# Kernel optimization log

Hardware: AMD Instinct MI355X
Metric: run time of the kernel (lower is better)

The kernel has to match this reference:

```python
import jax, jax.numpy as jnp
import numpy as np

N = 100_000          # NEURON_COUNT (scaled)
INPUT_SIZE = 1024    # input neurons occupy indices [0, INPUT_SIZE)
OUTPUT_SIZE = 256    # output neurons occupy indices [N-OUTPUT_SIZE, N)
E = 10_000_000       # SYNAPSE_RATIO * N
STEPS = 3


def setup_inputs() -> dict:
    key = jax.random.key(0)
    k1, k2, k3, k4, k5 = jax.random.split(key, 5)
    x = jax.random.normal(k1, (INPUT_SIZE,), dtype=jnp.float32)
    synapse_weights = jax.random.normal(k2, (E,), dtype=jnp.float32)
    neuron_biases = jax.random.normal(k3, (N - INPUT_SIZE,), dtype=jnp.float32)
    synapse_src = jax.random.randint(k4, (E,), 0, N, dtype=jnp.int64) if jax.config.jax_enable_x64 else jax.random.randint(k4, (E,), 0, N, dtype=jnp.int32)
    synapse_dst = jax.random.randint(k5, (E,), 0, N, dtype=jnp.int64) if jax.config.jax_enable_x64 else jax.random.randint(k5, (E,), 0, N, dtype=jnp.int32)
    return {
        "x": x,
        "synapse_weights": synapse_weights,
        "neuron_biases": neuron_biases,
        "synapse_src": synapse_src,
        "synapse_dst": synapse_dst,
    }


def reference(x, synapse_weights, neuron_biases, synapse_src, synapse_dst):
    # Initial state: zeros everywhere, inputs injected at the first INPUT_SIZE slots.
    v = jnp.zeros((N,), dtype=x.dtype).at[:INPUT_SIZE].set(x.reshape(-1))
    # tanh applied to all neurons except outputs (last OUTPUT_SIZE indices)
    tanh_mask = jnp.arange(N) < (N - OUTPUT_SIZE)
    for _ in range(STEPS):
        # vectorized gather-multiply-scatter: next[to] += v[from] * w  (one segment_sum)
        msg = v[synapse_src] * synapse_weights                       # [E]
        nxt = jax.ops.segment_sum(msg, synapse_dst, num_segments=N)  # [N]
        # biases added to all non-input neurons
        nxt = nxt.at[INPUT_SIZE:].add(neuron_biases)
        # tanh everywhere except output neurons
        v = jnp.where(tanh_mask, jnp.tanh(nxt), nxt)
    return v[N - OUTPUT_SIZE:]
```

## Files before the change

kernel.cpp:

```cpp
#include <hip/hip_runtime.h>

#define N_NEURONS   100000
#define INPUT_SIZE  1024
#define OUTPUT_SIZE 256
#define E_SYN       10000000
#define STEPS       3

#define RANGES      8
#define BIN         12500
#define SCAT_BLK    1024
#define CBLK        64
#define RG          8
#define RSL         (CBLK / RG)
#define CAP         1280000
#define VEC4        (E_SYN / 4)

#define CHK         1024
#define NCH         9766
#define PITER       (CHK / 256)
#define PW          4
#define HIST_GRID   ((NCH + PW - 1) / PW)
#define PART_GRID   ((NCH + PW - 1) / PW)
#define SCJ         ((NCH + 1023) / 1024)

__global__ void init_state(const float* __restrict__ x, float* __restrict__ v) {
    int i = blockIdx.x * blockDim.x + threadIdx.x;
    if (i < N_NEURONS) v[i] = (i < INPUT_SIZE) ? x[i] : 0.0f;
}

__global__ __launch_bounds__(256) void hist_kernel(const int* __restrict__ dst,
                                                   int* __restrict__ hist) {
    const int lane  = threadIdx.x & 63;
    const int wv    = threadIdx.x >> 6;
    const int chunk = blockIdx.x * PW + wv;
    if (chunk >= NCH) return;
    const int beg = chunk * CHK;
    const int4* dst4 = (const int4*)dst;
    int h = 0;
    for (int it = 0; it < PITER; ++it) {
        int e   = beg + (it * 64 + lane) * 4;
        bool ok = (e < E_SYN);
        int4 d4 = ok ? dst4[e >> 2] : make_int4(0, 0, 0, 0);
        unsigned long long okm = __ballot(ok);
        int rk[4] = {d4.x / BIN, d4.y / BIN, d4.z / BIN, d4.w / BIN};
#pragma unroll
        for (int k = 0; k < 4; ++k) {
            unsigned long long b0 = __ballot(rk[k] & 1);
            unsigned long long b1 = __ballot(rk[k] & 2);
            unsigned long long b2 = __ballot(rk[k] & 4);
            unsigned long long m = ((lane & 1) ? b0 : ~b0) &
                                   ((lane & 2) ? b1 : ~b1) &
                                   ((lane & 4) ? b2 : ~b2) & okm;
            h += __popcll(m);
        }
    }
    if (lane < RANGES) hist[(size_t)lane * NCH + chunk] = h;
}

__global__ __launch_bounds__(1024) void scan_kernel(const int* __restrict__ hist,
                                                    int* __restrict__ bases,
                                                    int* __restrict__ gcur) {
    const int r = blockIdx.x;
    const int t = threadIdx.x;
    const int lane = t & 63;
    const int wv   = t >> 6;
    int vals[SCJ];
    int s = 0;
#pragma unroll
    for (int j = 0; j < SCJ; ++j) {
        int idx = t * SCJ + j;
        int vv  = (idx < NCH) ? hist[(size_t)r * NCH + idx] : 0;
        vals[j] = vv;
        s += vv;
    }
    int x = s;
#pragma unroll
    for (int d = 1; d < 64; d <<= 1) {
        int y = __shfl_up(x, d, 64);
        if (lane >= d) x += y;
    }
    __shared__ int wsum[16];
    if (lane == 63) wsum[wv] = x;
    __syncthreads();
    if (wv == 0) {
        int y = (lane < 16) ? wsum[lane] : 0;
        int z = y;
#pragma unroll
        for (int d = 1; d < 16; d <<= 1) {
            int u = __shfl_up(z, d, 64);
            if (lane >= d) z += u;
        }
        if (lane < 16) wsum[lane] = z - y;
    }
    __syncthreads();
    int run = (x - s) + wsum[wv];
#pragma unroll
    for (int j = 0; j < SCJ; ++j) {
        int idx = t * SCJ + j;
        if (idx < NCH) bases[(size_t)r * NCH + idx] = r * CAP + run;
        run += vals[j];
    }
    if (t == 1023) gcur[r] = run;
}

__global__ __launch_bounds__(256) void partition_kernel(
        const float* __restrict__ w,
        const int*   __restrict__ src,
        const int*   __restrict__ dst,
        const int*   __restrict__ bases,
        int2* __restrict__ recs) {
    const int lane  = threadIdx.x & 63;
    const int wv    = threadIdx.x >> 6;
    const int chunk = blockIdx.x * PW + wv;
    if (chunk >= NCH) return;
    const unsigned long long ltmask = (1ull << lane) - 1ull;

    int cur = 0;
    if (lane < RANGES) cur = bases[(size_t)lane * NCH + chunk];

    const int beg = chunk * CHK;
    const int4* dst4 = (const int4*)dst;
    const int4* src4 = (const int4*)src;
    const int4* wq4  = (const int4*)w;

    for (int it = 0; it < PITER; ++it) {
        int e   = beg + (it * 64 + lane) * 4;
        bool ok = (e < E_SYN);
        int idx = e >> 2;
        int4 d4 = ok ? dst4[idx] : make_int4(0, 0, 0, 0);
        int4 s4 = ok ? src4[idx] : make_int4(0, 0, 0, 0);
        int4 q4 = ok ? wq4[idx]  : make_int4(0, 0, 0, 0);
        unsigned long long okm = __ballot(ok);
        int dd[4] = {d4.x, d4.y, d4.z, d4.w};
        int ss[4] = {s4.x, s4.y, s4.z, s4.w};
        int qq[4] = {q4.x, q4.y, q4.z, q4.w};
#pragma unroll
        for (int k = 0; k < 4; ++k) {
            int d = dd[k];
            int r = d / BIN;
            unsigned long long b0 = __ballot(r & 1);
            unsigned long long b1 = __ballot(r & 2);
            unsigned long long b2 = __ballot(r & 4);
            unsigned long long mym = ((r & 1) ? b0 : ~b0) &
                                     ((r & 2) ? b1 : ~b1) &
                                     ((r & 4) ? b2 : ~b2) & okm;
            int rank = __popcll(mym & ltmask);
            int gpos = __shfl(cur, r, 64) + rank;
            if (ok) recs[(size_t)gpos] =
                make_int2((ss[k] << 14) | (d - r * BIN), qq[k]);
            unsigned long long mm = ((lane & 1) ? b0 : ~b0) &
                                    ((lane & 2) ? b1 : ~b1) &
                                    ((lane & 4) ? b2 : ~b2) & okm;
            cur += __popcll(mm);
        }
    }
}

__global__ __launch_bounds__(SCAT_BLK) void scatter_sorted(
        const int2* __restrict__ recs,
        const int*  __restrict__ gcur,
        const float* __restrict__ v,
        float* __restrict__ partials) {
    __shared__ float bins[BIN];
    const int r = blockIdx.x / CBLK;
    const int c = blockIdx.x % CBLK;
    for (int j = threadIdx.x; j < BIN; j += SCAT_BLK) bins[j] = 0.0f;
    __syncthreads();

    const int cnt   = gcur[r];
    const int npair = cnt >> 1;
    const int4* base4 = (const int4*)(recs + (size_t)r * CAP);
    const int stride = CBLK * SCAT_BLK;
    int u = c * SCAT_BLK + threadIdx.x;
    for (; u + 3 * stride < npair; u += 4 * stride) {
        int4 a = base4[u];
        int4 b = base4[u + stride];
        int4 e = base4[u + 2 * stride];
        int4 f = base4[u + 3 * stride];
        float va0 = v[a.x >> 14];
        float va1 = v[a.z >> 14];
        float vb0 = v[b.x >> 14];
        float vb1 = v[b.z >> 14];
        float ve0 = v[e.x >> 14];
        float ve1 = v[e.z >> 14];
        float vf0 = v[f.x >> 14];
        float vf1 = v[f.z >> 14];
        atomicAdd(&bins[a.x & 16383], va0 * __int_as_float(a.y));
        atomicAdd(&bins[a.z & 16383], va1 * __int_as_float(a.w));
        atomicAdd(&bins[b.x & 16383], vb0 * __int_as_float(b.y));
        atomicAdd(&bins[b.z & 16383], vb1 * __int_as_float(b.w));
        atomicAdd(&bins[e.x & 16383], ve0 * __int_as_float(e.y));
        atomicAdd(&bins[e.z & 16383], ve1 * __int_as_float(e.w));
        atomicAdd(&bins[f.x & 16383], vf0 * __int_as_float(f.y));
        atomicAdd(&bins[f.z & 16383], vf1 * __int_as_float(f.w));
    }
    for (; u < npair; u += stride) {
        int4 a = base4[u];
        atomicAdd(&bins[a.x & 16383], v[a.x >> 14] * __int_as_float(a.y));
        atomicAdd(&bins[a.z & 16383], v[a.z >> 14] * __int_as_float(a.w));
    }
    if ((cnt & 1) && c == 0 && threadIdx.x == 0) {
        int2 p = recs[(size_t)r * CAP + cnt - 1];
        atomicAdd(&bins[p.x & 16383], v[p.x >> 14] * __int_as_float(p.y));
    }
    __syncthreads();
    float* o = partials + (size_t)(r * CBLK + c) * BIN;
    for (int j = threadIdx.x; j < BIN; j += SCAT_BLK) o[j] = bins[j];
}

__global__ void reduce_fused(const float* __restrict__ partials,
                             const float* __restrict__ bias,
                             float* __restrict__ v,
                             float* __restrict__ out,
                             int write_out) {
    int i4 = 4 * (blockIdx.x * blockDim.x + threadIdx.x);
    if (i4 >= N_NEURONS) return;
    const int r = i4 / BIN;
    const int j = i4 - r * BIN;
    const float* base = partials + (size_t)(r * CBLK) * BIN + j;
    float4 tot = {0.f, 0.f, 0.f, 0.f};
#pragma unroll 2
    for (int g = 0; g < RG; ++g) {
        float4 a = {0.f, 0.f, 0.f, 0.f};
#pragma unroll
        for (int cc = 0; cc < RSL; ++cc) {
            float4 p = *(const float4*)(base + (size_t)(g * RSL + cc) * BIN);
            a.x += p.x; a.y += p.y; a.z += p.z; a.w += p.w;
        }
        tot.x += a.x; tot.y += a.y; tot.z += a.z; tot.w += a.w;
    }
    float av[4] = {tot.x, tot.y, tot.z, tot.w};
#pragma unroll
    for (int k = 0; k < 4; ++k) {
        int i = i4 + k;
        float val = av[k] + ((i >= INPUT_SIZE) ? bias[i - INPUT_SIZE] : 0.0f);
        float nv  = (i < N_NEURONS - OUTPUT_SIZE) ? tanhf(val) : val;
        v[i] = nv;
        if (write_out && i >= N_NEURONS - OUTPUT_SIZE)
            out[i - (N_NEURONS - OUTPUT_SIZE)] = val;
    }
}

__global__ void scatter_binned(const float* __restrict__ w,
                               const int*   __restrict__ src,
                               const int*   __restrict__ dst,
                               const float* __restrict__ v,
                               float*       __restrict__ partials,
                               int C) {
    __shared__ float bins[BIN];
    const int r = blockIdx.x / C;
    const int c = blockIdx.x % C;
    const int lo = r * BIN;
    const int hi = lo + BIN;
    for (int j = threadIdx.x; j < BIN; j += blockDim.x) bins[j] = 0.0f;
    __syncthreads();
    const int4*   src4 = (const int4*)src;
    const int4*   dst4 = (const int4*)dst;
    const float4* w4v  = (const float4*)w;
    const int stride = C * blockDim.x;
    for (int u = c * blockDim.x + threadIdx.x; u < VEC4; u += stride) {
        const int4   s4 = src4[u];
        const int4   d4 = dst4[u];
        const float4 wv = w4v[u];
        int   s[4] = {s4.x, s4.y, s4.z, s4.w};
        int   d[4] = {d4.x, d4.y, d4.z, d4.w};
        float ww[4] = {wv.x, wv.y, wv.z, wv.w};
#pragma unroll
        for (int k = 0; k < 4; ++k)
            if (d[k] >= lo && d[k] < hi)
                atomicAdd(&bins[d[k] - lo], v[s[k]] * ww[k]);
    }
    __syncthreads();
    float* o = partials + ((size_t)(r * C + c)) * BIN;
    for (int j = threadIdx.x; j < BIN; j += blockDim.x) o[j] = bins[j];
}
__global__ void reduce_update_fb(const float* __restrict__ partials,
                                 const float* __restrict__ bias,
                                 float* __restrict__ v,
                                 float* __restrict__ out,
                                 int C, int write_out) {
    int i4 = 4 * (blockIdx.x * blockDim.x + threadIdx.x);
    if (i4 >= N_NEURONS) return;
    const int r = i4 / BIN;
    const int j = i4 - r * BIN;
    const float* base = partials + ((size_t)r * C) * BIN + j;
    float4 acc = {0.f, 0.f, 0.f, 0.f};
    for (int c = 0; c < C; ++c) {
        float4 p = *(const float4*)(base + (size_t)c * BIN);
        acc.x += p.x; acc.y += p.y; acc.z += p.z; acc.w += p.w;
    }
    float av[4] = {acc.x, acc.y, acc.z, acc.w};
#pragma unroll
    for (int k = 0; k < 4; ++k) {
        int i = i4 + k;
        float val = av[k] + ((i >= INPUT_SIZE) ? bias[i - INPUT_SIZE] : 0.0f);
        float nv  = (i < N_NEURONS - OUTPUT_SIZE) ? tanhf(val) : val;
        v[i] = nv;
        if (write_out && i >= N_NEURONS - OUTPUT_SIZE)
            out[i - (N_NEURONS - OUTPUT_SIZE)] = val;
    }
}

extern "C" void kernel_launch(void* const* d_in, const int* in_sizes, int n_in,
                              void* d_out, int out_size, void* d_ws, size_t ws_size,
                              hipStream_t stream) {
    const float* x    = (const float*)d_in[0];
    const float* w    = (const float*)d_in[1];
    const float* bias = (const float*)d_in[2];
    const int*   src  = (const int*)d_in[3];
    const int*   dst  = (const int*)d_in[4];
    float* out = (float*)d_out;

    const int blk = 256;
    const int grid_n   = (N_NEURONS + blk - 1) / blk;
    const int red_grid = (N_NEURONS / 4 + blk - 1) / blk;

    float* v        = (float*)d_ws;
    float* partials = v + N_NEURONS;
    int*   hist     = (int*)(partials + (size_t)RANGES * CBLK * BIN);
    int*   bases    = hist + (size_t)RANGES * NCH;
    int2*  recs     = (int2*)(bases + (size_t)RANGES * NCH);
    int*   gcur     = (int*)(recs + (size_t)RANGES * CAP);
    size_t need = (size_t)((char*)(gcur + RANGES) - (char*)d_ws);

    if (ws_size >= need) {
        init_state<<<grid_n, blk, 0, stream>>>(x, v);
        hist_kernel<<<HIST_GRID, 256, 0, stream>>>(dst, hist);
        scan_kernel<<<RANGES, 1024, 0, stream>>>(hist, bases, gcur);
        partition_kernel<<<PART_GRID, 256, 0, stream>>>(w, src, dst, bases, recs);
        for (int s = 0; s < STEPS; ++s) {
            scatter_sorted<<<RANGES * CBLK, SCAT_BLK, 0, stream>>>(
                recs, gcur, v, partials);
            reduce_fused<<<red_grid, blk, 0, stream>>>(
                partials, bias, v, out, s == STEPS - 1 ? 1 : 0);
        }
    } else {
        long C = (long)(ws_size / 4 / N_NEURONS) - 1;
        if (C > 64) C = 64;
        if (C < 1) C = 1;
        float* part_fb = v + N_NEURONS;
        init_state<<<grid_n, blk, 0, stream>>>(x, v);
        for (int s = 0; s < STEPS; ++s) {
            scatter_binned<<<RANGES * (int)C, SCAT_BLK, 0, stream>>>(
                w, src, dst, v, part_fb, (int)C);
            reduce_update_fb<<<red_grid, blk, 0, stream>>>(
                part_fb, bias, v, out, (int)C, s == STEPS - 1 ? 1 : 0);
        }
    }
}
```

Baseline: 384.5 us.

## Split partial reduction into two stages, halve chunk size, fuse init into histogram

The single reduce kernel, where each thread summed 64 partial rows serially, is replaced by two stages. A 2D-grid stage sums groups of 8 rows into an intermediate buffer, and a second stage sums the 8 groups and applies bias and tanh, which exposes more parallelism for the memory-bound reduction. The histogram/partition chunk size is halved so twice as many waves run. State initialization is folded into the histogram kernel to save a launch. The cost is an extra kernel per step, extra intermediate traffic, and more histogram/scan entries.

Result: no change. 388.1 us (+0.9%).

```diff
diff --git a/kernel.cpp b/kernel.cpp
--- a/kernel.cpp
+++ b/kernel.cpp
@@ -15,21 +15,19 @@
 #define CAP         1280000
 #define VEC4        (E_SYN / 4)
 
-#define CHK         1024
-#define NCH         9766
+#define CHK         512
+#define NCH         19532
 #define PITER       (CHK / 256)
 #define PW          4
 #define HIST_GRID   ((NCH + PW - 1) / PW)
-#define PART_GRID   ((NCH + PW - 1) / PW)
 #define SCJ         ((NCH + 1023) / 1024)
 
-__global__ void init_state(const float* __restrict__ x, float* __restrict__ v) {
-    int i = blockIdx.x * blockDim.x + threadIdx.x;
-    if (i < N_NEURONS) v[i] = (i < INPUT_SIZE) ? x[i] : 0.0f;
-}
-
-__global__ __launch_bounds__(256) void hist_kernel(const int* __restrict__ dst,
+__global__ __launch_bounds__(256) void hist_kernel(const float* __restrict__ x,
+                                                   float* __restrict__ v,
+                                                   const int* __restrict__ dst,
                                                    int* __restrict__ hist) {
+    const int gidx = blockIdx.x * 256 + threadIdx.x;
+    if (gidx < N_NEURONS) v[gidx] = (gidx < INPUT_SIZE) ? x[gidx] : 0.0f;
     const int lane  = threadIdx.x & 63;
     const int wv    = threadIdx.x >> 6;
     const int chunk = blockIdx.x * PW + wv;
@@ -208,28 +206,37 @@
     for (int j = threadIdx.x; j < BIN; j += SCAT_BLK) o[j] = bins[j];
 }
 
-__global__ void reduce_fused(const float* __restrict__ partials,
-                             const float* __restrict__ bias,
-                             float* __restrict__ v,
-                             float* __restrict__ out,
-                             int write_out) {
+__global__ void reduce_stage1(const float* __restrict__ partials,
+                              float* __restrict__ p2) {
     int i4 = 4 * (blockIdx.x * blockDim.x + threadIdx.x);
     if (i4 >= N_NEURONS) return;
+    const int g = blockIdx.y;
     const int r = i4 / BIN;
     const int j = i4 - r * BIN;
-    const float* base = partials + (size_t)(r * CBLK) * BIN + j;
-    float4 tot = {0.f, 0.f, 0.f, 0.f};
-#pragma unroll 2
+    const float* base = partials + ((size_t)(r * CBLK + g * RSL)) * BIN + j;
+    float4 acc = {0.f, 0.f, 0.f, 0.f};
+#pragma unroll
+    for (int c = 0; c < RSL; ++c) {
+        float4 p = *(const float4*)(base + (size_t)c * BIN);
+        acc.x += p.x; acc.y += p.y; acc.z += p.z; acc.w += p.w;
+    }
+    *(float4*)(p2 + (size_t)g * N_NEURONS + i4) = acc;
+}
+
+__global__ void reduce_stage2(const float* __restrict__ p2,
+                              const float* __restrict__ bias,
+                              float* __restrict__ v,
+                              float* __restrict__ out,
+                              int write_out) {
+    int i4 = 4 * (blockIdx.x * blockDim.x + threadIdx.x);
+    if (i4 >= N_NEURONS) return;
+    float4 acc = {0.f, 0.f, 0.f, 0.f};
+#pragma unroll
     for (int g = 0; g < RG; ++g) {
-        float4 a = {0.f, 0.f, 0.f, 0.f};
-#pragma unroll
-        for (int cc = 0; cc < RSL; ++cc) {
-            float4 p = *(const float4*)(base + (size_t)(g * RSL + cc) * BIN);
-            a.x += p.x; a.y += p.y; a.z += p.z; a.w += p.w;
-        }
-        tot.x += a.x; tot.y += a.y; tot.z += a.z; tot.w += a.w;
-    }
-    float av[4] = {tot.x, tot.y, tot.z, tot.w};
+        float4 p = *(const float4*)(p2 + (size_t)g * N_NEURONS + i4);
+        acc.x += p.x; acc.y += p.y; acc.z += p.z; acc.w += p.w;
+    }
+    float av[4] = {acc.x, acc.y, acc.z, acc.w};
 #pragma unroll
     for (int k = 0; k < 4; ++k) {
         int i = i4 + k;
@@ -241,6 +248,10 @@
     }
 }
 
+__global__ void init_state_fb(const float* __restrict__ x, float* __restrict__ v) {
+    int i = blockIdx.x * blockDim.x + threadIdx.x;
+    if (i < N_NEURONS) v[i] = (i < INPUT_SIZE) ? x[i] : 0.0f;
+}
 __global__ void scatter_binned(const float* __restrict__ w,
                                const int*   __restrict__ src,
                                const int*   __restrict__ dst,
@@ -317,29 +328,30 @@
 
     float* v        = (float*)d_ws;
     float* partials = v + N_NEURONS;
-    int*   hist     = (int*)(partials + (size_t)RANGES * CBLK * BIN);
+    float* p2       = partials + (size_t)RANGES * CBLK * BIN;
+    int*   hist     = (int*)(p2 + (size_t)RG * N_NEURONS);
     int*   bases    = hist + (size_t)RANGES * NCH;
-    int2*  recs     = (int2*)(bases + (size_t)RANGES * NCH);
-    int*   gcur     = (int*)(recs + (size_t)RANGES * CAP);
-    size_t need = (size_t)((char*)(gcur + RANGES) - (char*)d_ws);
+    int*   gcur     = bases + (size_t)RANGES * NCH;
+    int2*  recs     = (int2*)(gcur + RANGES);
+    size_t need = (size_t)((char*)(recs + (size_t)RANGES * CAP) - (char*)d_ws);
 
     if (ws_size >= need) {
-        init_state<<<grid_n, blk, 0, stream>>>(x, v);
-        hist_kernel<<<HIST_GRID, 256, 0, stream>>>(dst, hist);
+        hist_kernel<<<HIST_GRID, 256, 0, stream>>>(x, v, dst, hist);
         scan_kernel<<<RANGES, 1024, 0, stream>>>(hist, bases, gcur);
-        partition_kernel<<<PART_GRID, 256, 0, stream>>>(w, src, dst, bases, recs);
+        partition_kernel<<<HIST_GRID, 256, 0, stream>>>(w, src, dst, bases, recs);
         for (int s = 0; s < STEPS; ++s) {
             scatter_sorted<<<RANGES * CBLK, SCAT_BLK, 0, stream>>>(
                 recs, gcur, v, partials);
-            reduce_fused<<<red_grid, blk, 0, stream>>>(
-                partials, bias, v, out, s == STEPS - 1 ? 1 : 0);
+            reduce_stage1<<<dim3(red_grid, RG), blk, 0, stream>>>(partials, p2);
+            reduce_stage2<<<red_grid, blk, 0, stream>>>(
+                p2, bias, v, out, s == STEPS - 1 ? 1 : 0);
         }
     } else {
         long C = (long)(ws_size / 4 / N_NEURONS) - 1;
         if (C > 64) C = 64;
         if (C < 1) C = 1;
         float* part_fb = v + N_NEURONS;
-        init_state<<<grid_n, blk, 0, stream>>>(x, v);
+        init_state_fb<<<grid_n, blk, 0, stream>>>(x, v);
         for (int s = 0; s < STEPS; ++s) {
             scatter_binned<<<RANGES * (int)C, SCAT_BLK, 0, stream>>>(
                 w, src, dst, v, part_fb, (int)C);
```
